# Kernel tuning notes

Hardware: AMD Instinct MI355X
Metric: run time of the kernel (lower is better)

## Reference

```python
import jax, jax.numpy as jnp
import numpy as np

N = 100000
E = 6400000
GAMMA = 1.0
SUPPORT = 0.05


def cohesion_kernel(q, h):
    # piecewise Akinci cohesion kernel (Cd normalization is unused in the original)
    qm1_3_q3 = (q - 1.0) ** 3 * q ** 3
    k1 = 128.0 * qm1_3_q3 + 1.0   # q <= 0.5
    k2 = 64.0 * qm1_3_q3           # q > 0.5
    return -jnp.where(q <= 0.5, k1, k2)


def kernel_gradient(q, dist, h):
    # 2D Wendland C2 kernel gradient: W = 7/(pi h^2) (1-q)^4 (1+4q)
    C = 7.0 / (np.pi * h ** 2)
    dWdq = C * (-20.0 * q * jnp.clip(1.0 - q, 0.0, None) ** 3) / h
    return dWdq[:, None] * dist  # [E,2]


def setup_inputs() -> dict:
    key = jax.random.key(0)
    k1, k2, k3, k4, k5, k6, k7 = jax.random.split(key, 7)
    neighbors = jnp.stack([
        jax.random.randint(k1, (E,), 0, N),
        jax.random.randint(k2, (E,), 0, N),
    ], axis=0)  # [2,E] int
    fluidAreas = jax.random.uniform(k3, (N,), dtype=jnp.float32)
    fluidDensities = jax.random.uniform(k4, (N,), dtype=jnp.float32) + 0.5  # avoid div-by-0
    fluidRestDensity = jax.random.uniform(k5, (N,), dtype=jnp.float32) + 0.5
    fluidRadialDistances = jax.random.uniform(k6, (E,), dtype=jnp.float32)  # q in [0,1]
    fluidDistances = jax.random.normal(k7, (E, 2), dtype=jnp.float32)
    # normalize to unit direction vectors as in the SPH pipeline
    fluidDistances = fluidDistances / (jnp.linalg.norm(fluidDistances, axis=1, keepdims=True) + 1e-7)
    return {
        'neighbors': neighbors,
        'fluidAreas': fluidAreas,
        'fluidDensities': fluidDensities,
        'fluidRestDensity': fluidRestDensity,
        'fluidRadialDistances': fluidRadialDistances,
        'fluidDistances': fluidDistances,
    }


def reference(neighbors, fluidAreas, fluidDensities, fluidRestDensity,
              fluidRadialDistances, fluidDistances):
    i = neighbors[0]
    j = neighbors[1]

    # computeNormalFunction
    fac_n = fluidAreas[j] / fluidDensities[j]                  # [E]
    grad = kernel_gradient(fluidRadialDistances, fluidDistances, SUPPORT)  # [E,2]
    normals = SUPPORT * jax.ops.segment_sum(fac_n[:, None] * grad, i, num_segments=N)  # [N,2]

    # computeCurvatureForce
    curvature = -GAMMA * jax.ops.segment_sum(normals[i] - normals[j], i, num_segments=N)

    # computeCohesionForce
    fac_c = fluidAreas[j] * fluidRestDensity[j]                # [E]
    kern = cohesion_kernel(fluidRadialDistances, SUPPORT)      # [E]
    cohesion = -GAMMA * jax.ops.segment_sum((fac_c * kern)[:, None] * fluidDistances, i, num_segments=N)

    # both forces are accumulated into fluidAcceleration
    return curvature + cohesion
```

## Files before the change

### kernel.cpp

```cpp
#include <hip/hip_runtime.h>

constexpr int N_PART = 100000;
constexpr int N_EDGE = 6400000;
constexpr float SUPPORT = 0.05f;
constexpr float PI_F = 3.14159265358979323846f;

constexpr int CH_LOG2 = 13;
constexpr int CH      = 1 << CH_LOG2;
constexpr int NCH     = (N_EDGE + CH - 1) / CH;
constexpr int BIN_LOG2 = 13;
constexpr int BINSZ   = 1 << BIN_LOG2;
constexpr int NBIN    = (N_PART + BINSZ - 1) / BINSZ;
constexpr int G_MAX   = 39;
constexpr int ST_NW   = 16;

__global__ __launch_bounds__(1024) void l1_sort(
    const int* __restrict__ nb,
    const float* __restrict__ areas,
    const float* __restrict__ dens,
    const float* __restrict__ rest,
    const float* __restrict__ q,
    const float2* __restrict__ dist,
    unsigned* __restrict__ gpack,
    float2* __restrict__ gpay1,
    float2* __restrict__ gpay2,
    unsigned* __restrict__ btab)
{
    __shared__ float4  rec[CH];
    __shared__ unsigned hist[ST_NW * NBIN];
    __shared__ unsigned curw[ST_NW * NBIN];
    __shared__ unsigned base[NBIN + 1];

    const int t   = blockIdx.x;
    const int c0  = t * CH;
    const int len = min(CH, N_EDGE - c0);
    const int tid = threadIdx.x;
    const int wid = tid >> 6;

    for (int k = tid; k < ST_NW * NBIN; k += 1024) hist[k] = 0u;
    __syncthreads();

    for (int idx = tid; idx < len; idx += 1024) {
        unsigned i = (unsigned)nb[c0 + idx];
        atomicAdd(&hist[wid * NBIN + (i >> BIN_LOG2)], 1u);
    }
    __syncthreads();

    if (tid == 0) {
        unsigned run = 0;
        for (int b = 0; b < NBIN; ++b) {
            base[b] = run;
            for (int w = 0; w < ST_NW; ++w) {
                curw[w * NBIN + b] = run;
                run += hist[w * NBIN + b];
            }
        }
        base[NBIN] = run;
    }
    __syncthreads();
    if (tid < NBIN)  btab[t * 16 + tid]  = base[tid];
    if (tid == NBIN) btab[t * 16 + NBIN] = (unsigned)len;

    for (int idx = tid; idx < len; idx += 1024) {
        unsigned i = (unsigned)nb[c0 + idx];
        unsigned j = (unsigned)nb[N_EDGE + c0 + idx];
        float   qq = q[c0 + idx];
        float2  d  = dist[c0 + idx];
        unsigned bin = i >> BIN_LOG2;
        unsigned r = atomicAdd(&curw[wid * NBIN + bin], 1u) & (CH - 1);
        unsigned pack = ((i & (BINSZ - 1)) << 17) | j;
        rec[r] = make_float4(__uint_as_float(pack), qq, d.x, d.y);
    }
    __syncthreads();

    const float Cw = 7.0f / (PI_F * SUPPORT * SUPPORT);
    for (int p = tid; p < len; p += 1024) {
        float4 rc = rec[p];
        unsigned pack = __float_as_uint(rc.x);
        unsigned j = pack & 0x1FFFFu;
        float qq = rc.y;
        float dx = rc.z, dy = rc.w;

        float omq  = fmaxf(1.0f - qq, 0.0f);
        float dWdq = Cw * (-20.0f * qq * omq * omq * omq) * (1.0f / SUPPORT);
        float s    = SUPPORT * (areas[j] / dens[j]) * dWdq;

        float qm1  = qq - 1.0f;
        float tt   = qm1 * qm1 * qm1 * qq * qq * qq;
        float kern = (qq <= 0.5f) ? fmaf(128.0f, tt, 1.0f) : 64.0f * tt;
        float fc   = areas[j] * rest[j] * kern;

        int o = c0 + p;
        gpack[o] = pack;
        gpay1[o] = make_float2(s * dx, s * dy);
        gpay2[o] = make_float2(fc * dx, fc * dy);
    }
}

__global__ __launch_bounds__(512) void passB(
    const unsigned* __restrict__ btab,
    const unsigned* __restrict__ gpack,
    const float2* __restrict__ gpay1,
    float2* __restrict__ partials,
    int G)
{
    __shared__ float acc[2 * BINSZ];
    const int b = blockIdx.x % NBIN;
    const int g = blockIdx.x / NBIN;

    for (int k = threadIdx.x; k < 2 * BINSZ; k += 512) acc[k] = 0.0f;
    __syncthreads();

    const int t0 = (int)((long long)g * NCH / G);
    const int t1 = (int)((long long)(g + 1) * NCH / G);
    for (int t = t0; t < t1; ++t) {
        const int c0  = t * CH;
        const unsigned ln = min(btab[t * 16 + NBIN], (unsigned)CH);
        unsigned sb = min(btab[t * 16 + b], ln);
        unsigned se = min(btab[t * 16 + b + 1], ln);
        for (unsigned k = sb + threadIdx.x; k < se; k += 512) {
            int o = c0 + (int)k;
            unsigned pk = gpack[o];
            float2 p = gpay1[o];
            unsigned loc = (pk >> 17) & (BINSZ - 1);
            atomicAdd(&acc[2 * loc],     p.x);
            atomicAdd(&acc[2 * loc + 1], p.y);
        }
    }
    __syncthreads();

    float2* __restrict__ dst = partials + (size_t)g * (NBIN * BINSZ) + (size_t)b * BINSZ;
    const float2* __restrict__ src = (const float2*)acc;
    for (int k = threadIdx.x; k < BINSZ; k += 512) dst[k] = src[k];
}

__global__ __launch_bounds__(512) void passD(
    const unsigned* __restrict__ btab,
    const unsigned* __restrict__ gpack,
    const float2* __restrict__ gpay2,
    const float2* __restrict__ normals,
    float2* __restrict__ partials,
    int G)
{
    __shared__ float acc[2 * BINSZ];
    const int b = blockIdx.x % NBIN;
    const int g = blockIdx.x / NBIN;

    for (int k = threadIdx.x; k < 2 * BINSZ; k += 512) acc[k] = 0.0f;
    __syncthreads();

    const int gbase = b * BINSZ;
    const int t0 = (int)((long long)g * NCH / G);
    const int t1 = (int)((long long)(g + 1) * NCH / G);
    for (int t = t0; t < t1; ++t) {
        const int c0  = t * CH;
        const unsigned ln = min(btab[t * 16 + NBIN], (unsigned)CH);
        unsigned sb = min(btab[t * 16 + b], ln);
        unsigned se = min(btab[t * 16 + b + 1], ln);
        for (unsigned k = sb + threadIdx.x; k < se; k += 512) {
            int o = c0 + (int)k;
            unsigned pk = gpack[o];
            float2 coh = gpay2[o];
            unsigned loc = (pk >> 17) & (BINSZ - 1);
            unsigned j   = min(pk & 0x1FFFFu, (unsigned)(N_PART - 1));
            unsigned ii  = min((unsigned)(gbase + loc), (unsigned)(N_PART - 1));
            float2 nj = normals[j];
            float2 ni = normals[ii];
            atomicAdd(&acc[2 * loc],     nj.x - ni.x + coh.x);
            atomicAdd(&acc[2 * loc + 1], nj.y - ni.y + coh.y);
        }
    }
    __syncthreads();

    float2* __restrict__ dst = partials + (size_t)g * (NBIN * BINSZ) + (size_t)b * BINSZ;
    const float2* __restrict__ src = (const float2*)acc;
    for (int k = threadIdx.x; k < BINSZ; k += 512) dst[k] = src[k];
}

__global__ __launch_bounds__(256) void reduceG(
    const float2* __restrict__ partials, float2* __restrict__ dst, int G)
{
    int p = blockIdx.x * blockDim.x + threadIdx.x;
    if (p >= N_PART) return;
    float ax = 0.0f, ay = 0.0f;
    for (int g = 0; g < G; ++g) {
        float2 v = partials[(size_t)g * (NBIN * BINSZ) + p];
        ax += v.x; ay += v.y;
    }
    dst[p] = make_float2(ax, ay);
}

constexpr int FB_BSZ_LOG2 = 13;
constexpr int FB_BSZ   = 1 << FB_BSZ_LOG2;
constexpr int FB_NBINS = (N_PART + FB_BSZ - 1) / FB_BSZ;
constexpr int FB_NP_PAD = FB_NBINS * FB_BSZ;
constexpr int FB_C_TARGET = 39;

__global__ __launch_bounds__(1024) void fb_pass1_binned(
    const int* __restrict__ nb, const float* __restrict__ areas,
    const float* __restrict__ dens, const float* __restrict__ q,
    const float2* __restrict__ dist, float* __restrict__ partials, int C)
{
    __shared__ float lds[2 * FB_BSZ];
    const int b = blockIdx.x % FB_NBINS;
    const int c = blockIdx.x / FB_NBINS;
    for (int k = threadIdx.x; k < 2 * FB_BSZ; k += blockDim.x) lds[k] = 0.0f;
    __syncthreads();
    const int start = (int)((long long)c       * (N_EDGE / 4) / C) * 4;
    const int end   = (int)((long long)(c + 1) * (N_EDGE / 4) / C) * 4;
    const int4* __restrict__ nb4 = (const int4*)nb;
    const float Cw = 7.0f / (PI_F * SUPPORT * SUPPORT);
    for (int e = start + (int)threadIdx.x * 4; e < end; e += (int)blockDim.x * 4) {
        int4 iq = nb4[e >> 2];
        #pragma unroll
        for (int k = 0; k < 4; ++k) {
            int iv = (k == 0) ? iq.x : (k == 1) ? iq.y : (k == 2) ? iq.z : iq.w;
            if ((iv >> FB_BSZ_LOG2) == b) {
                int ee = e + k;
                int j  = nb[N_EDGE + ee];
                float qq  = q[ee];
                float fac = areas[j] / dens[j];
                float omq  = fmaxf(1.0f - qq, 0.0f);
                float dWdq = Cw * (-20.0f * qq * omq * omq * omq) * (1.0f / SUPPORT);
                float s = SUPPORT * fac * dWdq;
                float2 d = dist[ee];
                int loc = (iv & (FB_BSZ - 1)) << 1;
                atomicAdd(&lds[loc],     s * d.x);
                atomicAdd(&lds[loc + 1], s * d.y);
            }
        }
    }
    __syncthreads();
    float2* __restrict__ dst = (float2*)partials + (size_t)c * FB_NP_PAD + (size_t)b * FB_BSZ;
    const float2* __restrict__ src = (const float2*)lds;
    for (int k = threadIdx.x; k < FB_BSZ; k += blockDim.x) dst[k] = src[k];
}

__global__ __launch_bounds__(1024) void fb_pass2_binned(
    const int* __restrict__ nb, const float* __restrict__ areas,
    const float* __restrict__ rest, const float* __restrict__ q,
    const float2* __restrict__ dist, const float2* __restrict__ normals,
    float* __restrict__ partials, int C)
{
    __shared__ float lds[2 * FB_BSZ];
    const int b = blockIdx.x % FB_NBINS;
    const int c = blockIdx.x / FB_NBINS;
    for (int k = threadIdx.x; k < 2 * FB_BSZ; k += blockDim.x) lds[k] = 0.0f;
    __syncthreads();
    const int start = (int)((long long)c       * (N_EDGE / 4) / C) * 4;
    const int end   = (int)((long long)(c + 1) * (N_EDGE / 4) / C) * 4;
    const int4* __restrict__ nb4 = (const int4*)nb;
    for (int e = start + (int)threadIdx.x * 4; e < end; e += (int)blockDim.x * 4) {
        int4 iq = nb4[e >> 2];
        #pragma unroll
        for (int k = 0; k < 4; ++k) {
            int iv = (k == 0) ? iq.x : (k == 1) ? iq.y : (k == 2) ? iq.z : iq.w;
            if ((iv >> FB_BSZ_LOG2) == b) {
                int ee = e + k;
                int j  = nb[N_EDGE + ee];
                float2 ni = normals[iv];
                float2 nj = normals[j];
                float qq  = q[ee];
                float fc  = areas[j] * rest[j];
                float qm1 = qq - 1.0f;
                float t   = qm1 * qm1 * qm1 * qq * qq * qq;
                float kern = (qq <= 0.5f) ? fmaf(128.0f, t, 1.0f) : 64.0f * t;
                float2 d = dist[ee];
                int loc = (iv & (FB_BSZ - 1)) << 1;
                atomicAdd(&lds[loc],     -(ni.x - nj.x) + fc * kern * d.x);
                atomicAdd(&lds[loc + 1], -(ni.y - nj.y) + fc * kern * d.y);
            }
        }
    }
    __syncthreads();
    float2* __restrict__ dst = (float2*)partials + (size_t)c * FB_NP_PAD + (size_t)b * FB_BSZ;
    const float2* __restrict__ src = (const float2*)lds;
    for (int k = threadIdx.x; k < FB_BSZ; k += blockDim.x) dst[k] = src[k];
}

__global__ __launch_bounds__(256) void fb_reduce_partials(
    const float* __restrict__ partials, float* __restrict__ dst, int C)
{
    int p = blockIdx.x * blockDim.x + threadIdx.x;
    if (p >= N_PART) return;
    const float2* __restrict__ p2 = (const float2*)partials;
    float ax = 0.0f, ay = 0.0f;
    for (int c = 0; c < C; ++c) {
        float2 v = p2[(size_t)c * FB_NP_PAD + p];
        ax += v.x; ay += v.y;
    }
    ((float2*)dst)[p] = make_float2(ax, ay);
}

__global__ __launch_bounds__(256) void fb_zero2(float* __restrict__ a,
                                                float* __restrict__ b, int n) {
    int idx = blockIdx.x * blockDim.x + threadIdx.x;
    if (idx < n) { a[idx] = 0.0f; b[idx] = 0.0f; }
}

__global__ __launch_bounds__(256) void fb_pass1_atomic(
    const int* __restrict__ nb, const float* __restrict__ areas,
    const float* __restrict__ dens, const float* __restrict__ q,
    const float2* __restrict__ dist, float* __restrict__ normals)
{
    int e = blockIdx.x * blockDim.x + threadIdx.x;
    if (e >= N_EDGE) return;
    int i = nb[e];
    int j = nb[N_EDGE + e];
    float qq  = q[e];
    float fac = areas[j] / dens[j];
    const float Cw = 7.0f / (PI_F * SUPPORT * SUPPORT);
    float omq  = fmaxf(1.0f - qq, 0.0f);
    float dWdq = Cw * (-20.0f * qq * omq * omq * omq) * (1.0f / SUPPORT);
    float s = SUPPORT * fac * dWdq;
    float2 d = dist[e];
    atomicAdd(&normals[2 * i],     s * d.x);
    atomicAdd(&normals[2 * i + 1], s * d.y);
}

__global__ __launch_bounds__(256) void fb_pass2_atomic(
    const int* __restrict__ nb, const float* __restrict__ areas,
    const float* __restrict__ rest, const float* __restrict__ q,
    const float2* __restrict__ dist, const float2* __restrict__ normals,
    float* __restrict__ out)
{
    int e = blockIdx.x * blockDim.x + threadIdx.x;
    if (e >= N_EDGE) return;
    int i = nb[e];
    int j = nb[N_EDGE + e];
    float2 ni = normals[i];
    float2 nj = normals[j];
    float qq  = q[e];
    float fc  = areas[j] * rest[j];
    float qm1 = qq - 1.0f;
    float t   = qm1 * qm1 * qm1 * qq * qq * qq;
    float kern = (qq <= 0.5f) ? fmaf(128.0f, t, 1.0f) : 64.0f * t;
    float2 d = dist[e];
    atomicAdd(&out[2 * i],     -(ni.x - nj.x) + fc * kern * d.x);
    atomicAdd(&out[2 * i + 1], -(ni.y - nj.y) + fc * kern * d.y);
}

extern "C" void kernel_launch(void* const* d_in, const int* in_sizes, int n_in,
                              void* d_out, int out_size, void* d_ws, size_t ws_size,
                              hipStream_t stream) {
    const int*   nb    = (const int*)d_in[0];
    const float* areas = (const float*)d_in[1];
    const float* dens  = (const float*)d_in[2];
    const float* rest  = (const float*)d_in[3];
    const float* q     = (const float*)d_in[4];
    const float* dist  = (const float*)d_in[5];
    float* out = (float*)d_out;

    size_t off = 0;
    auto take = [&](size_t bytes) { size_t o = off; off += (bytes + 255) & ~(size_t)255; return o; };
    size_t o_pack    = take((size_t)N_EDGE * sizeof(unsigned));
    size_t o_pay1    = take((size_t)N_EDGE * sizeof(float2));
    size_t o_pay2    = take((size_t)N_EDGE * sizeof(float2));
    size_t o_btab    = take((size_t)NCH * 16 * sizeof(unsigned));
    size_t o_normals = take((size_t)N_PART * sizeof(float2));
    size_t base_need = off;
    const size_t per_g = (size_t)(NBIN * BINSZ) * sizeof(float2);

    int G = 0;
    if (ws_size > base_need) {
        G = (int)((ws_size - base_need) / per_g);
        if (G > G_MAX) G = G_MAX;
    }

    char* ws = (char*)d_ws;

    if (G >= 6) {
        unsigned* gpack   = (unsigned*)(ws + o_pack);
        float2*   gpay1   = (float2*)(ws + o_pay1);
        float2*   gpay2   = (float2*)(ws + o_pay2);
        unsigned* btab    = (unsigned*)(ws + o_btab);
        float2*   normals = (float2*)(ws + o_normals);
        float2*   partials= (float2*)(ws + base_need);

        l1_sort<<<NCH, 1024, 0, stream>>>(
            nb, areas, dens, rest, q, (const float2*)dist,
            gpack, gpay1, gpay2, btab);
        passB<<<NBIN * G, 512, 0, stream>>>(btab, gpack, gpay1, partials, G);
        reduceG<<<(N_PART + 255) / 256, 256, 0, stream>>>(partials, normals, G);
        passD<<<NBIN * G, 512, 0, stream>>>(btab, gpack, gpay2, normals, partials, G);
        reduceG<<<(N_PART + 255) / 256, 256, 0, stream>>>(partials, (float2*)out, G);
        return;
    }

    const size_t normals_pad = 1 << 20;
    float* normals  = (float*)d_ws;
    float* partials = (float*)((char*)d_ws + normals_pad);
    const size_t per_chunk = (size_t)FB_NP_PAD * 2 * sizeof(float);
    int C = 0;
    if (ws_size > normals_pad) {
        C = (int)((ws_size - normals_pad) / per_chunk);
        if (C > FB_C_TARGET) C = FB_C_TARGET;
    }

    if (C >= 4) {
        const int grid = FB_NBINS * C;
        fb_pass1_binned<<<grid, 1024, 0, stream>>>(
            nb, areas, dens, q, (const float2*)dist, partials, C);
        fb_reduce_partials<<<(N_PART + 255) / 256, 256, 0, stream>>>(partials, normals, C);
        fb_pass2_binned<<<grid, 1024, 0, stream>>>(
            nb, areas, rest, q, (const float2*)dist, (const float2*)normals, partials, C);
        fb_reduce_partials<<<(N_PART + 255) / 256, 256, 0, stream>>>(partials, out, C);
    } else {
        const int nv = 2 * N_PART;
        fb_zero2<<<(nv + 255) / 256, 256, 0, stream>>>(normals, out, nv);
        const int blocks = (N_EDGE + 255) / 256;
        fb_pass1_atomic<<<blocks, 256, 0, stream>>>(
            nb, areas, dens, q, (const float2*)dist, normals);
        fb_pass2_atomic<<<blocks, 256, 0, stream>>>(
            nb, areas, rest, q, (const float2*)dist, (const float2*)normals, out);
    }
}
```

Measured before the change: 450.9 us.

## Halve sort chunk size, split shared arrays to SoA, wave-per-chunk accumulation

The sort kernel now uses 4096-edge chunks with 512 threads and 8 histogram waves, which doubles the number of sort blocks and lowers shared memory use per block. Shared records and accumulators are split into separate arrays to avoid strided/bank-conflicted float4/float2 access. In passB/passD each wave processes a different chunk with 64-lane strides instead of the whole block sharing one chunk's short bin segment, reducing idle lanes. Risk: more chunks means larger btab and more per-chunk overhead in the pass kernels.

```diff
diff --git a/kernel.cpp b/kernel.cpp
--- a/kernel.cpp
+++ b/kernel.cpp
@@ -5,16 +5,16 @@
 constexpr float SUPPORT = 0.05f;
 constexpr float PI_F = 3.14159265358979323846f;
 
-constexpr int CH_LOG2 = 13;
+constexpr int CH_LOG2 = 12;
 constexpr int CH      = 1 << CH_LOG2;
 constexpr int NCH     = (N_EDGE + CH - 1) / CH;
 constexpr int BIN_LOG2 = 13;
 constexpr int BINSZ   = 1 << BIN_LOG2;
 constexpr int NBIN    = (N_PART + BINSZ - 1) / BINSZ;
 constexpr int G_MAX   = 39;
-constexpr int ST_NW   = 16;
-
-__global__ __launch_bounds__(1024) void l1_sort(
+constexpr int ST_NW   = 8;
+
+__global__ __launch_bounds__(512) void l1_sort(
     const int* __restrict__ nb,
     const float* __restrict__ areas,
     const float* __restrict__ dens,
@@ -26,7 +26,10 @@
     float2* __restrict__ gpay2,
     unsigned* __restrict__ btab)
 {
-    __shared__ float4  rec[CH];
+    __shared__ unsigned rec_pack[CH];
+    __shared__ float    rec_q[CH];
+    __shared__ float    rec_dx[CH];
+    __shared__ float    rec_dy[CH];
     __shared__ unsigned hist[ST_NW * NBIN];
     __shared__ unsigned curw[ST_NW * NBIN];
     __shared__ unsigned base[NBIN + 1];
@@ -37,10 +40,10 @@
     const int tid = threadIdx.x;
     const int wid = tid >> 6;
 
-    for (int k = tid; k < ST_NW * NBIN; k += 1024) hist[k] = 0u;
-    __syncthreads();
-
-    for (int idx = tid; idx < len; idx += 1024) {
+    for (int k = tid; k < ST_NW * NBIN; k += 512) hist[k] = 0u;
+    __syncthreads();
+
+    for (int idx = tid; idx < len; idx += 512) {
         unsigned i = (unsigned)nb[c0 + idx];
         atomicAdd(&hist[wid * NBIN + (i >> BIN_LOG2)], 1u);
     }
@@ -61,25 +64,26 @@
     if (tid < NBIN)  btab[t * 16 + tid]  = base[tid];
     if (tid == NBIN) btab[t * 16 + NBIN] = (unsigned)len;
 
-    for (int idx = tid; idx < len; idx += 1024) {
+    for (int idx = tid; idx < len; idx += 512) {
         unsigned i = (unsigned)nb[c0 + idx];
         unsigned j = (unsigned)nb[N_EDGE + c0 + idx];
         float   qq = q[c0 + idx];
         float2  d  = dist[c0 + idx];
         unsigned bin = i >> BIN_LOG2;
         unsigned r = atomicAdd(&curw[wid * NBIN + bin], 1u) & (CH - 1);
-        unsigned pack = ((i & (BINSZ - 1)) << 17) | j;
-        rec[r] = make_float4(__uint_as_float(pack), qq, d.x, d.y);
+        rec_pack[r] = ((i & (BINSZ - 1)) << 17) | j;
+        rec_q[r]    = qq;
+        rec_dx[r]   = d.x;
+        rec_dy[r]   = d.y;
     }
     __syncthreads();
 
     const float Cw = 7.0f / (PI_F * SUPPORT * SUPPORT);
-    for (int p = tid; p < len; p += 1024) {
-        float4 rc = rec[p];
-        unsigned pack = __float_as_uint(rc.x);
+    for (int p = tid; p < len; p += 512) {
+        unsigned pack = rec_pack[p];
+        float qq = rec_q[p];
+        float dx = rec_dx[p], dy = rec_dy[p];
         unsigned j = pack & 0x1FFFFu;
-        float qq = rc.y;
-        float dx = rc.z, dy = rc.w;
 
         float omq  = fmaxf(1.0f - qq, 0.0f);
         float dWdq = Cw * (-20.0f * qq * omq * omq * omq) * (1.0f / SUPPORT);
@@ -104,34 +108,37 @@
     float2* __restrict__ partials,
     int G)
 {
-    __shared__ float acc[2 * BINSZ];
+    __shared__ float accx[BINSZ];
+    __shared__ float accy[BINSZ];
     const int b = blockIdx.x % NBIN;
     const int g = blockIdx.x / NBIN;
-
-    for (int k = threadIdx.x; k < 2 * BINSZ; k += 512) acc[k] = 0.0f;
+    const int wave = threadIdx.x >> 6;
+    const int lane = threadIdx.x & 63;
+
+    for (int k = threadIdx.x; k < BINSZ; k += 512) { accx[k] = 0.0f; accy[k] = 0.0f; }
     __syncthreads();
 
     const int t0 = (int)((long long)g * NCH / G);
     const int t1 = (int)((long long)(g + 1) * NCH / G);
-    for (int t = t0; t < t1; ++t) {
+    for (int t = t0 + wave; t < t1; t += 8) {
         const int c0  = t * CH;
         const unsigned ln = min(btab[t * 16 + NBIN], (unsigned)CH);
         unsigned sb = min(btab[t * 16 + b], ln);
         unsigned se = min(btab[t * 16 + b + 1], ln);
-        for (unsigned k = sb + threadIdx.x; k < se; k += 512) {
+        for (unsigned k = sb + lane; k < se; k += 64) {
             int o = c0 + (int)k;
             unsigned pk = gpack[o];
             float2 p = gpay1[o];
             unsigned loc = (pk >> 17) & (BINSZ - 1);
-            atomicAdd(&acc[2 * loc],     p.x);
-            atomicAdd(&acc[2 * loc + 1], p.y);
+            atomicAdd(&accx[loc], p.x);
+            atomicAdd(&accy[loc], p.y);
         }
     }
     __syncthreads();
 
     float2* __restrict__ dst = partials + (size_t)g * (NBIN * BINSZ) + (size_t)b * BINSZ;
-    const float2* __restrict__ src = (const float2*)acc;
-    for (int k = threadIdx.x; k < BINSZ; k += 512) dst[k] = src[k];
+    for (int k = threadIdx.x; k < BINSZ; k += 512)
+        dst[k] = make_float2(accx[k], accy[k]);
 }
 
 __global__ __launch_bounds__(512) void passD(
@@ -142,22 +149,25 @@
     float2* __restrict__ partials,
     int G)
 {
-    __shared__ float acc[2 * BINSZ];
+    __shared__ float accx[BINSZ];
+    __shared__ float accy[BINSZ];
     const int b = blockIdx.x % NBIN;
     const int g = blockIdx.x / NBIN;
-
-    for (int k = threadIdx.x; k < 2 * BINSZ; k += 512) acc[k] = 0.0f;
+    const int wave = threadIdx.x >> 6;
+    const int lane = threadIdx.x & 63;
+
+    for (int k = threadIdx.x; k < BINSZ; k += 512) { accx[k] = 0.0f; accy[k] = 0.0f; }
     __syncthreads();
 
     const int gbase = b * BINSZ;
     const int t0 = (int)((long long)g * NCH / G);
     const int t1 = (int)((long long)(g + 1) * NCH / G);
-    for (int t = t0; t < t1; ++t) {
+    for (int t = t0 + wave; t < t1; t += 8) {
         const int c0  = t * CH;
         const unsigned ln = min(btab[t * 16 + NBIN], (unsigned)CH);
         unsigned sb = min(btab[t * 16 + b], ln);
         unsigned se = min(btab[t * 16 + b + 1], ln);
-        for (unsigned k = sb + threadIdx.x; k < se; k += 512) {
+        for (unsigned k = sb + lane; k < se; k += 64) {
             int o = c0 + (int)k;
             unsigned pk = gpack[o];
             float2 coh = gpay2[o];
@@ -166,15 +176,15 @@
             unsigned ii  = min((unsigned)(gbase + loc), (unsigned)(N_PART - 1));
             float2 nj = normals[j];
             float2 ni = normals[ii];
-            atomicAdd(&acc[2 * loc],     nj.x - ni.x + coh.x);
-            atomicAdd(&acc[2 * loc + 1], nj.y - ni.y + coh.y);
+            atomicAdd(&accx[loc], nj.x - ni.x + coh.x);
+            atomicAdd(&accy[loc], nj.y - ni.y + coh.y);
         }
     }
     __syncthreads();
 
     float2* __restrict__ dst = partials + (size_t)g * (NBIN * BINSZ) + (size_t)b * BINSZ;
-    const float2* __restrict__ src = (const float2*)acc;
-    for (int k = threadIdx.x; k < BINSZ; k += 512) dst[k] = src[k];
+    for (int k = threadIdx.x; k < BINSZ; k += 512)
+        dst[k] = make_float2(accx[k], accy[k]);
 }
 
 __global__ __launch_bounds__(256) void reduceG(
@@ -377,7 +387,7 @@
         float2*   normals = (float2*)(ws + o_normals);
         float2*   partials= (float2*)(ws + base_need);
 
-        l1_sort<<<NCH, 1024, 0, stream>>>(
+        l1_sort<<<NCH, 512, 0, stream>>>(
             nb, areas, dens, rest, q, (const float2*)dist,
             gpack, gpay1, gpay2, btab);
         passB<<<NBIN * G, 512, 0, stream>>>(btab, gpack, gpay1, partials, G);
```

After: 432.1 us. 4.2% less time.
